# Kernel optimization log

Hardware: AMD Instinct MI355X
Metric: run time of the kernel (lower is better)

## Reference

```python
import jax, jax.numpy as jnp
import numpy as np

NH, NKV, HD = 16, 4, 64   # n_heads, n_kv_heads, head_dim
N_REP = NH // NKV
EPS = 1e-6


def rms_norm(x, w):
    var = jnp.mean(x.astype(jnp.float32) ** 2, axis=-1, keepdims=True)
    return (x.astype(jnp.float32) * jax.lax.rsqrt(var + EPS)).astype(x.dtype) * w


def rotate_half(x):
    x1, x2 = jnp.split(x, 2, axis=-1)
    return jnp.concatenate([-x2, x1], axis=-1)


def setup_inputs() -> dict:
    key = jax.random.key(0)
    ks = jax.random.split(key, 6)
    B, S, H = 2, 2048, 2048
    x = jax.random.normal(ks[0], (B, S, H), dtype=jnp.float32)
    # RoPE tables [S, HD]
    inv_freq = 1.0 / (10000.0 ** (jnp.arange(0, HD, 2, dtype=jnp.float32) / HD))
    freqs = jnp.arange(S, dtype=jnp.float32)[:, None] * inv_freq[None, :]
    emb = jnp.concatenate([freqs, freqs], axis=-1)
    cos, sin = jnp.cos(emb), jnp.sin(emb)
    scale = 0.02
    wq = jax.random.normal(ks[1], (H, NH * HD), dtype=jnp.float32) * scale
    wk = jax.random.normal(ks[2], (H, NKV * HD), dtype=jnp.float32) * scale
    wv = jax.random.normal(ks[3], (H, NKV * HD), dtype=jnp.float32) * scale
    wo = jax.random.normal(ks[4], (NH * HD, H), dtype=jnp.float32) * scale
    q_norm_w = jnp.ones((HD,), dtype=jnp.float32)
    k_norm_w = jnp.ones((HD,), dtype=jnp.float32)
    return {"x": x, "cos": cos, "sin": sin, "wq": wq, "wk": wk, "wv": wv,
            "wo": wo, "q_norm_w": q_norm_w, "k_norm_w": k_norm_w}


def reference(x, cos, sin, wq, wk, wv, wo, q_norm_w, k_norm_w):
    B, S, H = x.shape
    # QKV projections + per-head RMSNorm on q/k
    q = rms_norm((x @ wq).reshape(B, S, NH, HD), q_norm_w)
    k = rms_norm((x @ wk).reshape(B, S, NKV, HD), k_norm_w)
    v = (x @ wv).reshape(B, S, NKV, HD)
    # RoPE (broadcast over heads)
    c = cos[None, :S, None, :]
    s = sin[None, :S, None, :]
    q = q * c + rotate_half(q) * s
    k = k * c + rotate_half(k) * s
    # prefill with S == window_size: no KV eviction, T == S -> causal mask
    k = jnp.repeat(k, N_REP, axis=2)  # [B,S,NH,HD]
    v = jnp.repeat(v, N_REP, axis=2)
    scores = jnp.einsum('bqhd,bkhd->bhqk', q, k) / jnp.sqrt(jnp.float32(HD))
    causal = jnp.triu(jnp.full((S, S), -jnp.inf, dtype=scores.dtype), 1)
    scores = scores + causal
    attn = jax.nn.softmax(scores.astype(jnp.float32), axis=-1).astype(q.dtype)
    out = jnp.einsum('bhqk,bkhd->bqhd', attn, v).reshape(B, S, NH * HD)
    return out @ wo
```

## Files before the change

### kernel.cpp

```cpp
#include <hip/hip_runtime.h>

typedef float floatx4 __attribute__((ext_vector_type(4)));
typedef __bf16 bfx8 __attribute__((ext_vector_type(8)));
typedef __bf16 bfx4 __attribute__((ext_vector_type(4)));

constexpr int B_ = 2, S_ = 2048, H_ = 2048, NH_ = 16, NKV_ = 4, HD_ = 64;
constexpr int M_ = B_ * S_;
constexpr int NQKV_ = NH_ * HD_ + 2 * NKV_ * HD_;
constexpr int HQ_ = NH_ * HD_;
constexpr int XP_ = 2112;
constexpr int AP_ = 1088;
constexpr int VP_ = 2112;
constexpr int QKV_ELEMS_ = M_ * NQKV_;
constexpr float QSCL_ = 0.125f * 1.44269504088896340736f;

#define GLB(p) ((const __attribute__((address_space(1))) void*)(p))
#define LDS(p) ((__attribute__((address_space(3))) void*)(p))

__global__ __launch_bounds__(256) void prep_kernel(const float* __restrict__ x,
                                                   const float* __restrict__ wq,
                                                   const float* __restrict__ wk,
                                                   const float* __restrict__ wv,
                                                   const float* __restrict__ wo,
                                                   __bf16* __restrict__ xbf,
                                                   __bf16* __restrict__ wqkvT,
                                                   __bf16* __restrict__ woT) {
  __shared__ float tile[32][33];
  int bid = blockIdx.x;
  if (bid < M_) {
    const float4* s = (const float4*)(x + (size_t)bid * H_);
    __bf16* d = xbf + (size_t)bid * XP_;
#pragma unroll
    for (int i = 0; i < 2; i++) {
      int c = i * 256 + threadIdx.x;
      float4 v = s[c];
      bfx4 o;
      o[0] = (__bf16)v.x; o[1] = (__bf16)v.y; o[2] = (__bf16)v.z; o[3] = (__bf16)v.w;
      *(bfx4*)(d + c * 4) = o;
    }
    return;
  }
  bid -= M_;
  const float* src; __bf16* dst; int N, dstOff, pitch, nbx;
  if (bid < 2048)      { src = wq; dst = wqkvT; N = 1024; dstOff = 0;    pitch = XP_; nbx = 32; }
  else if (bid < 2560) { bid -= 2048; src = wk; dst = wqkvT; N = 256; dstOff = 1024; pitch = XP_; nbx = 8; }
  else if (bid < 3072) { bid -= 2560; src = wv; dst = wqkvT; N = 256; dstOff = 1280; pitch = XP_; nbx = 8; }
  else                 { bid -= 3072; src = wo; dst = woT;   N = 2048; dstOff = 0;   pitch = AP_; nbx = 64; }
  int n0 = (bid % nbx) * 32, k0 = (bid / nbx) * 32;
  int tx = threadIdx.x & 31, ty = threadIdx.x >> 5;
#pragma unroll
  for (int r = 0; r < 32; r += 8)
    tile[ty + r][tx] = src[(size_t)(k0 + ty + r) * N + n0 + tx];
  __syncthreads();
#pragma unroll
  for (int r = 0; r < 32; r += 8)
    dst[(size_t)(n0 + ty + r + dstOff) * pitch + k0 + tx] = (__bf16)tile[tx][ty + r];
}

__global__ __launch_bounds__(512) void gemm_bf16_f32(const __bf16* __restrict__ A,
                                                     const __bf16* __restrict__ Bt,
                                                     float* __restrict__ C,
                                                     int M, int N, int K,
                                                     int lda, int ldb, int ldc,
                                                     unsigned long long cstride) {
  __shared__ __align__(16) __bf16 As[256 * 64];
  __shared__ __align__(16) __bf16 Bs[128 * 64];
  int wid = threadIdx.x >> 6, lane = threadIdx.x & 63;
  int l15 = lane & 15, quad = lane >> 4;
  int wm = (wid >> 1) * 64, wn = (wid & 1) * 64;
  int m0 = blockIdx.y * 256, n0 = blockIdx.x * 128;
  int kb0 = blockIdx.z * K;
  C += (size_t)blockIdx.z * cstride;
  int srow_off = lane >> 3;
  int gphys = lane & 7;
  floatx4 acc[4][4] = {};
  for (int kb = kb0; kb < kb0 + K; kb += 64) {
#pragma unroll
    for (int j = 0; j < 4; j++) {
      int rbase = j * 64 + wid * 8;
      int row = rbase + srow_off;
      int glog = gphys ^ (row & 7);
      const __bf16* ga = &A[(size_t)(m0 + row) * lda + kb + glog * 8];
      __builtin_amdgcn_global_load_lds(GLB(ga), LDS(&As[rbase * 64]), 16, 0, 0);
    }
#pragma unroll
    for (int j = 0; j < 2; j++) {
      int rbase = j * 64 + wid * 8;
      int row = rbase + srow_off;
      int glog = gphys ^ (row & 7);
      const __bf16* gb = &Bt[(size_t)(n0 + row) * ldb + kb + glog * 8];
      __builtin_amdgcn_global_load_lds(GLB(gb), LDS(&Bs[rbase * 64]), 16, 0, 0);
    }
    __syncthreads();
#pragma unroll
    for (int kk = 0; kk < 64; kk += 32) {
      int cgq = (kk >> 3) + quad;
      bfx8 af[4], bfr[4];
#pragma unroll
      for (int mi = 0; mi < 4; mi++) {
        int row = wm + mi * 16 + l15;
        af[mi] = *(const bfx8*)&As[row * 64 + (cgq ^ (row & 7)) * 8];
      }
#pragma unroll
      for (int ni = 0; ni < 4; ni++) {
        int row = wn + ni * 16 + l15;
        bfr[ni] = *(const bfx8*)&Bs[row * 64 + (cgq ^ (row & 7)) * 8];
      }
#pragma unroll
      for (int mi = 0; mi < 4; mi++)
#pragma unroll
        for (int ni = 0; ni < 4; ni++)
          acc[mi][ni] = __builtin_amdgcn_mfma_f32_16x16x32_bf16(af[mi], bfr[ni], acc[mi][ni], 0, 0, 0);
    }
    __syncthreads();
  }
#pragma unroll
  for (int mi = 0; mi < 4; mi++)
#pragma unroll
    for (int ni = 0; ni < 4; ni++) {
      int row = m0 + wm + mi * 16 + quad * 4;
      int coln = n0 + wn + ni * 16 + l15;
#pragma unroll
      for (int r = 0; r < 4; r++)
        C[(size_t)(row + r) * ldc + coln] = acc[mi][ni][r];
    }
}

__global__ __launch_bounds__(256) void norm_rope_kernel(const float* __restrict__ qkv,
                                                        const float* __restrict__ cosT,
                                                        const float* __restrict__ sinT,
                                                        const float* __restrict__ qw,
                                                        const float* __restrict__ kw,
                                                        __bf16* __restrict__ Qo,
                                                        __bf16* __restrict__ Ko,
                                                        __bf16* __restrict__ VTo) {
  int s = blockIdx.x, b = blockIdx.y;
  int wid = threadIdx.x >> 6, lane = threadIdx.x & 63;
  const float* rowp = qkv + (size_t)(b * S_ + s) * NQKV_;
  const float* rowp2 = rowp + QKV_ELEMS_;
  float c = cosT[s * HD_ + lane];
  float sn = sinT[s * HD_ + lane];
#pragma unroll
  for (int it = 0; it < 5; it++) {
    int hh = it * 4 + wid;
    int idx = hh * 64 + lane;
    float v = rowp[idx] + rowp2[idx];
    float ss = v * v;
#pragma unroll
    for (int off = 1; off < 64; off <<= 1) ss += __shfl_xor(ss, off);
    float rs = rsqrtf(ss * (1.0f / 64.0f) + 1e-6f);
    const float* w = (hh < 16) ? qw : kw;
    float nv = v * rs * w[lane];
    float other = __shfl_xor(nv, 32);
    float rot = (lane < 32) ? -other : other;
    float outv = nv * c + rot * sn;
    if (hh < 16)
      Qo[(((size_t)b * NH_ + hh) * S_ + s) * HD_ + lane] = (__bf16)(outv * QSCL_);
    else
      Ko[(((size_t)b * NKV_ + (hh - 16)) * S_ + s) * HD_ + lane] = (__bf16)outv;
  }
  {
    int idx = (20 + wid) * 64 + lane;
    float v = rowp[idx] + rowp2[idx];
    VTo[(((size_t)b * NKV_ + wid) * HD_ + lane) * VP_ + s] = (__bf16)v;
  }
}

__global__ __launch_bounds__(256, 4) void attn_kernel(const __bf16* __restrict__ Q,
                                                      const __bf16* __restrict__ Kc,
                                                      const __bf16* __restrict__ VT,
                                                      __bf16* __restrict__ Ob) {
  int px = blockIdx.x, h = blockIdx.y, b = blockIdx.z;
  int u = (px + 2 * (h & 7)) & 31;
  int qt = (((h >> 3) ^ b) & 1) ? (31 - u) : u;
  int wid = threadIdx.x >> 6, lane = threadIdx.x & 63;
  int l15 = lane & 15, quad = lane >> 4;
  int q0 = qt * 64 + wid * 16;
  int kvh = h >> 2;
  const __bf16* Qh = Q + (((size_t)b * NH_ + h) * S_ + q0) * HD_;
  const __bf16* Kh = Kc + ((size_t)b * NKV_ + kvh) * S_ * HD_;
  const __bf16* Vh = VT + ((size_t)b * NKV_ + kvh) * (size_t)HD_ * VP_;
  __shared__ __align__(16) __bf16 Ks[64][72];
  __shared__ __align__(16) __bf16 Vs[64][72];
  __shared__ __align__(16) __bf16 Pst[4][16][72];
  __bf16 (*P)[72] = Pst[wid];

  int srow = threadIdx.x >> 3;
  int scol = (threadIdx.x & 7) * 8;

  bfx8 qf0, qf1;
  {
    const __bf16* qp = Qh + l15 * HD_ + quad * 8;
    qf0 = *(const bfx8*)qp;
    qf1 = *(const bfx8*)(qp + 32);
  }
  floatx4 oacc[4] = {};
  float ps = 0.f;
  int ntiles = qt + 1;
  bfx8 kpre0, kpre1, vpre0, vpre1;
  kpre0 = *(const bfx8*)&Kh[(size_t)srow * HD_ + scol];
  kpre1 = *(const bfx8*)&Kh[(size_t)(srow + 32) * HD_ + scol];
  vpre0 = *(const bfx8*)&Vh[(size_t)srow * VP_ + scol];
  vpre1 = *(const bfx8*)&Vh[(size_t)(srow + 32) * VP_ + scol];
  for (int kt = 0; kt < ntiles; kt++) {
    int kv0 = kt * 64;
    __syncthreads();
    *(bfx8*)&Ks[srow][scol] = kpre0;
    *(bfx8*)&Ks[srow + 32][scol] = kpre1;
    *(bfx8*)&Vs[srow][scol] = vpre0;
    *(bfx8*)&Vs[srow + 32][scol] = vpre1;
    __syncthreads();
    if (kt + 1 < ntiles) {
      int kn = kv0 + 64;
      kpre0 = *(const bfx8*)&Kh[(size_t)(kn + srow) * HD_ + scol];
      kpre1 = *(const bfx8*)&Kh[(size_t)(kn + srow + 32) * HD_ + scol];
      vpre0 = *(const bfx8*)&Vh[(size_t)srow * VP_ + kn + scol];
      vpre1 = *(const bfx8*)&Vh[(size_t)(srow + 32) * VP_ + kn + scol];
    }
    floatx4 sf[4];
    __builtin_amdgcn_s_setprio(1);
#pragma unroll
    for (int nt = 0; nt < 4; nt++) {
      bfx8 kf0 = *(const bfx8*)&Ks[nt * 16 + l15][quad * 8];
      bfx8 kf1 = *(const bfx8*)&Ks[nt * 16 + l15][32 + quad * 8];
      floatx4 z = {0.f, 0.f, 0.f, 0.f};
      z = __builtin_amdgcn_mfma_f32_16x16x32_bf16(kf0, qf0, z, 0, 0, 0);
      sf[nt] = __builtin_amdgcn_mfma_f32_16x16x32_bf16(kf1, qf1, z, 0, 0, 0);
    }
    __builtin_amdgcn_s_setprio(0);
    if (kt + 1 < ntiles) {
#pragma unroll
      for (int nt = 0; nt < 4; nt++) {
        bfx4 pk;
#pragma unroll
        for (int r = 0; r < 4; r++) {
          float p = exp2f(sf[nt][r]);
          ps += p;
          pk[r] = (__bf16)p;
        }
        *(bfx4*)&P[l15][nt * 16 + quad * 4] = pk;
      }
    } else {
      int dq = q0 - kv0;
#pragma unroll
      for (int nt = 0; nt < 4; nt++) {
        bfx4 pk;
#pragma unroll
        for (int r = 0; r < 4; r++) {
          int kvrel = nt * 16 + quad * 4 + r;
          float p = exp2f(sf[nt][r]);
          p = (kvrel - l15 > dq) ? 0.f : p;
          ps += p;
          pk[r] = (__bf16)p;
        }
        *(bfx4*)&P[l15][nt * 16 + quad * 4] = pk;
      }
    }
    bfx8 pa0 = *(const bfx8*)&P[l15][quad * 8];
    bfx8 pa1 = *(const bfx8*)&P[l15][32 + quad * 8];
    __builtin_amdgcn_s_setprio(1);
#pragma unroll
    for (int ot = 0; ot < 4; ot++) {
      bfx8 vf0 = *(const bfx8*)&Vs[ot * 16 + l15][quad * 8];
      bfx8 vf1 = *(const bfx8*)&Vs[ot * 16 + l15][32 + quad * 8];
      oacc[ot] = __builtin_amdgcn_mfma_f32_16x16x32_bf16(pa0, vf0, oacc[ot], 0, 0, 0);
      oacc[ot] = __builtin_amdgcn_mfma_f32_16x16x32_bf16(pa1, vf1, oacc[ot], 0, 0, 0);
    }
    __builtin_amdgcn_s_setprio(0);
  }
  ps += __shfl_xor(ps, 16);
  ps += __shfl_xor(ps, 32);
  float rl[4];
#pragma unroll
  for (int r = 0; r < 4; r++) rl[r] = 1.0f / __shfl(ps, quad * 4 + r);
#pragma unroll
  for (int ot = 0; ot < 4; ot++)
#pragma unroll
    for (int r = 0; r < 4; r++) {
      float val = oacc[ot][r] * rl[r];
      Ob[((size_t)b * S_ + q0 + quad * 4 + r) * AP_ + h * HD_ + ot * 16 + l15] = (__bf16)val;
    }
}

extern "C" void kernel_launch(void* const* d_in, const int* in_sizes, int n_in,
                              void* d_out, int out_size, void* d_ws, size_t ws_size,
                              hipStream_t stream) {
  const float* x   = (const float*)d_in[0];
  const float* cosT = (const float*)d_in[1];
  const float* sinT = (const float*)d_in[2];
  const float* wq  = (const float*)d_in[3];
  const float* wk  = (const float*)d_in[4];
  const float* wv  = (const float*)d_in[5];
  const float* wo  = (const float*)d_in[6];
  const float* qw  = (const float*)d_in[7];
  const float* kw  = (const float*)d_in[8];
  float* out = (float*)d_out;

  char* w = (char*)d_ws;
  __bf16* xbf   = (__bf16*)(w);
  __bf16* Qb    = (__bf16*)(w);
  __bf16* Kb    = (__bf16*)(w + 8388608);
  __bf16* VTb   = (__bf16*)(w + 10485760);
  __bf16* wqkvT = (__bf16*)(w + 17301504);
  __bf16* woT   = (__bf16*)(w + 23789568);
  float*  qkv   = (float*) (w + 28246016);
  __bf16* attnO = (__bf16*)(w + 28246016);

  prep_kernel<<<M_ + 5120, 256, 0, stream>>>(x, wq, wk, wv, wo, xbf, wqkvT, woT);
  gemm_bf16_f32<<<dim3(NQKV_ / 128, M_ / 256, 2), 512, 0, stream>>>(
      xbf, wqkvT, qkv, M_, NQKV_, H_ / 2, XP_, XP_, NQKV_, (unsigned long long)QKV_ELEMS_);
  norm_rope_kernel<<<dim3(S_, B_), 256, 0, stream>>>(qkv, cosT, sinT, qw, kw, Qb, Kb, VTb);
  attn_kernel<<<dim3(32, NH_, B_), 256, 0, stream>>>(Qb, Kb, VTb, attnO);
  gemm_bf16_f32<<<dim3(H_ / 128, M_ / 256, 1), 512, 0, stream>>>(
      attnO, woT, out, M_, H_, HQ_, AP_, AP_, H_, 0ull);
}
```

Baseline: 225.9 us.

## Enlarge attention query tile to 128 rows with XOR-swizzled K/V shared memory

```diff
diff --git a/kernel.cpp b/kernel.cpp
--- a/kernel.cpp
+++ b/kernel.cpp
@@ -166,119 +166,146 @@
   }
 }
 
-__global__ __launch_bounds__(256, 4) void attn_kernel(const __bf16* __restrict__ Q,
+__global__ __launch_bounds__(256, 2) void attn_kernel(const __bf16* __restrict__ Q,
                                                       const __bf16* __restrict__ Kc,
                                                       const __bf16* __restrict__ VT,
                                                       __bf16* __restrict__ Ob) {
   int px = blockIdx.x, h = blockIdx.y, b = blockIdx.z;
-  int u = (px + 2 * (h & 7)) & 31;
-  int qt = (((h >> 3) ^ b) & 1) ? (31 - u) : u;
+  int u = (px + 2 * (h & 7)) & 15;
+  int qt = (((h >> 3) ^ b) & 1) ? (15 - u) : u;
   int wid = threadIdx.x >> 6, lane = threadIdx.x & 63;
   int l15 = lane & 15, quad = lane >> 4;
-  int q0 = qt * 64 + wid * 16;
+  int q0w = qt * 128 + wid * 32;
   int kvh = h >> 2;
-  const __bf16* Qh = Q + (((size_t)b * NH_ + h) * S_ + q0) * HD_;
+  const __bf16* Qh = Q + (((size_t)b * NH_ + h) * S_ + q0w) * HD_;
   const __bf16* Kh = Kc + ((size_t)b * NKV_ + kvh) * S_ * HD_;
   const __bf16* Vh = VT + ((size_t)b * NKV_ + kvh) * (size_t)HD_ * VP_;
-  __shared__ __align__(16) __bf16 Ks[64][72];
-  __shared__ __align__(16) __bf16 Vs[64][72];
-  __shared__ __align__(16) __bf16 Pst[4][16][72];
+  __shared__ __align__(16) __bf16 Ks[64][64];
+  __shared__ __align__(16) __bf16 Vs[64][64];
+  __shared__ __align__(16) __bf16 Pst[4][32][72];
   __bf16 (*P)[72] = Pst[wid];
 
   int srow = threadIdx.x >> 3;
-  int scol = (threadIdx.x & 7) * 8;
-
-  bfx8 qf0, qf1;
+  int sg   = threadIdx.x & 7;
+  int pcol = (sg ^ (srow & 7)) * 8;
+
+  bfx8 qf0, qf1, qf2, qf3;
   {
     const __bf16* qp = Qh + l15 * HD_ + quad * 8;
     qf0 = *(const bfx8*)qp;
     qf1 = *(const bfx8*)(qp + 32);
-  }
-  floatx4 oacc[4] = {};
-  float ps = 0.f;
-  int ntiles = qt + 1;
+    qf2 = *(const bfx8*)(qp + 16 * HD_);
+    qf3 = *(const bfx8*)(qp + 16 * HD_ + 32);
+  }
+  floatx4 oacc0[4] = {}, oacc1[4] = {};
+  float ps0 = 0.f, ps1 = 0.f;
+  int ntiles = 2 * qt + 2;
+  int ktm = 2 * qt + (wid >> 1);
+  int dq0 = (wid & 1) * 32;
+  int dq1 = dq0 + 16;
+
   bfx8 kpre0, kpre1, vpre0, vpre1;
-  kpre0 = *(const bfx8*)&Kh[(size_t)srow * HD_ + scol];
-  kpre1 = *(const bfx8*)&Kh[(size_t)(srow + 32) * HD_ + scol];
-  vpre0 = *(const bfx8*)&Vh[(size_t)srow * VP_ + scol];
-  vpre1 = *(const bfx8*)&Vh[(size_t)(srow + 32) * VP_ + scol];
+  kpre0 = *(const bfx8*)&Kh[(size_t)srow * HD_ + sg * 8];
+  kpre1 = *(const bfx8*)&Kh[(size_t)(srow + 32) * HD_ + sg * 8];
+  vpre0 = *(const bfx8*)&Vh[(size_t)srow * VP_ + sg * 8];
+  vpre1 = *(const bfx8*)&Vh[(size_t)(srow + 32) * VP_ + sg * 8];
   for (int kt = 0; kt < ntiles; kt++) {
     int kv0 = kt * 64;
     __syncthreads();
-    *(bfx8*)&Ks[srow][scol] = kpre0;
-    *(bfx8*)&Ks[srow + 32][scol] = kpre1;
-    *(bfx8*)&Vs[srow][scol] = vpre0;
-    *(bfx8*)&Vs[srow + 32][scol] = vpre1;
+    *(bfx8*)&Ks[srow][pcol] = kpre0;
+    *(bfx8*)&Ks[srow + 32][pcol] = kpre1;
+    *(bfx8*)&Vs[srow][pcol] = vpre0;
+    *(bfx8*)&Vs[srow + 32][pcol] = vpre1;
     __syncthreads();
     if (kt + 1 < ntiles) {
       int kn = kv0 + 64;
-      kpre0 = *(const bfx8*)&Kh[(size_t)(kn + srow) * HD_ + scol];
-      kpre1 = *(const bfx8*)&Kh[(size_t)(kn + srow + 32) * HD_ + scol];
-      vpre0 = *(const bfx8*)&Vh[(size_t)srow * VP_ + kn + scol];
-      vpre1 = *(const bfx8*)&Vh[(size_t)(srow + 32) * VP_ + kn + scol];
-    }
-    floatx4 sf[4];
-    __builtin_amdgcn_s_setprio(1);
+      kpre0 = *(const bfx8*)&Kh[(size_t)(kn + srow) * HD_ + sg * 8];
+      kpre1 = *(const bfx8*)&Kh[(size_t)(kn + srow + 32) * HD_ + sg * 8];
+      vpre0 = *(const bfx8*)&Vh[(size_t)srow * VP_ + kn + sg * 8];
+      vpre1 = *(const bfx8*)&Vh[(size_t)(srow + 32) * VP_ + kn + sg * 8];
+    }
+    if (kt > ktm) continue;
+
+    floatx4 sf0[4], sf1[4];
 #pragma unroll
     for (int nt = 0; nt < 4; nt++) {
-      bfx8 kf0 = *(const bfx8*)&Ks[nt * 16 + l15][quad * 8];
-      bfx8 kf1 = *(const bfx8*)&Ks[nt * 16 + l15][32 + quad * 8];
-      floatx4 z = {0.f, 0.f, 0.f, 0.f};
-      z = __builtin_amdgcn_mfma_f32_16x16x32_bf16(kf0, qf0, z, 0, 0, 0);
-      sf[nt] = __builtin_amdgcn_mfma_f32_16x16x32_bf16(kf1, qf1, z, 0, 0, 0);
-    }
-    __builtin_amdgcn_s_setprio(0);
-    if (kt + 1 < ntiles) {
+      int r = nt * 16 + l15;
+      int g0 = (quad ^ (r & 7)) * 8;
+      bfx8 kf0 = *(const bfx8*)&Ks[r][g0];
+      bfx8 kf1 = *(const bfx8*)&Ks[r][g0 ^ 32];
+      floatx4 z0 = {0.f, 0.f, 0.f, 0.f}, z1 = {0.f, 0.f, 0.f, 0.f};
+      z0 = __builtin_amdgcn_mfma_f32_16x16x32_bf16(kf0, qf0, z0, 0, 0, 0);
+      sf0[nt] = __builtin_amdgcn_mfma_f32_16x16x32_bf16(kf1, qf1, z0, 0, 0, 0);
+      z1 = __builtin_amdgcn_mfma_f32_16x16x32_bf16(kf0, qf2, z1, 0, 0, 0);
+      sf1[nt] = __builtin_amdgcn_mfma_f32_16x16x32_bf16(kf1, qf3, z1, 0, 0, 0);
+    }
+    if (kt < ktm) {
 #pragma unroll
       for (int nt = 0; nt < 4; nt++) {
-        bfx4 pk;
+        bfx4 pk0, pk1;
 #pragma unroll
         for (int r = 0; r < 4; r++) {
-          float p = exp2f(sf[nt][r]);
-          ps += p;
-          pk[r] = (__bf16)p;
+          float p0 = exp2f(sf0[nt][r]);
+          float p1 = exp2f(sf1[nt][r]);
+          ps0 += p0; ps1 += p1;
+          pk0[r] = (__bf16)p0; pk1[r] = (__bf16)p1;
         }
-        *(bfx4*)&P[l15][nt * 16 + quad * 4] = pk;
+        *(bfx4*)&P[l15][nt * 16 + quad * 4] = pk0;
+        *(bfx4*)&P[16 + l15][nt * 16 + quad * 4] = pk1;
       }
     } else {
-      int dq = q0 - kv0;
 #pragma unroll
       for (int nt = 0; nt < 4; nt++) {
-        bfx4 pk;
+        bfx4 pk0, pk1;
 #pragma unroll
         for (int r = 0; r < 4; r++) {
           int kvrel = nt * 16 + quad * 4 + r;
-          float p = exp2f(sf[nt][r]);
-          p = (kvrel - l15 > dq) ? 0.f : p;
-          ps += p;
-          pk[r] = (__bf16)p;
+          float p0 = exp2f(sf0[nt][r]);
+          float p1 = exp2f(sf1[nt][r]);
+          p0 = (kvrel - l15 > dq0) ? 0.f : p0;
+          p1 = (kvrel - l15 > dq1) ? 0.f : p1;
+          ps0 += p0; ps1 += p1;
+          pk0[r] = (__bf16)p0; pk1[r] = (__bf16)p1;
         }
-        *(bfx4*)&P[l15][nt * 16 + quad * 4] = pk;
+        *(bfx4*)&P[l15][nt * 16 + quad * 4] = pk0;
+        *(bfx4*)&P[16 + l15][nt * 16 + quad * 4] = pk1;
       }
     }
-    bfx8 pa0 = *(const bfx8*)&P[l15][quad * 8];
-    bfx8 pa1 = *(const bfx8*)&P[l15][32 + quad * 8];
-    __builtin_amdgcn_s_setprio(1);
+    bfx8 pa00 = *(const bfx8*)&P[l15][quad * 8];
+    bfx8 pa01 = *(const bfx8*)&P[l15][32 + quad * 8];
+    bfx8 pa10 = *(const bfx8*)&P[16 + l15][quad * 8];
+    bfx8 pa11 = *(const bfx8*)&P[16 + l15][32 + quad * 8];
 #pragma unroll
     for (int ot = 0; ot < 4; ot++) {
-      bfx8 vf0 = *(const bfx8*)&Vs[ot * 16 + l15][quad * 8];
-      bfx8 vf1 = *(const bfx8*)&Vs[ot * 16 + l15][32 + quad * 8];
-      oacc[ot] = __builtin_amdgcn_mfma_f32_16x16x32_bf16(pa0, vf0, oacc[ot], 0, 0, 0);
-      oacc[ot] = __builtin_amdgcn_mfma_f32_16x16x32_bf16(pa1, vf1, oacc[ot], 0, 0, 0);
-    }
-    __builtin_amdgcn_s_setprio(0);
-  }
-  ps += __shfl_xor(ps, 16);
-  ps += __shfl_xor(ps, 32);
-  float rl[4];
-#pragma unroll
-  for (int r = 0; r < 4; r++) rl[r] = 1.0f / __shfl(ps, quad * 4 + r);
+      int d = ot * 16 + l15;
+      int g0 = (quad ^ (d & 7)) * 8;
+      bfx8 vf0 = *(const bfx8*)&Vs[d][g0];
+      bfx8 vf1 = *(const bfx8*)&Vs[d][g0 ^ 32];
+      oacc0[ot] = __builtin_amdgcn_mfma_f32_16x16x32_bf16(pa00, vf0, oacc0[ot], 0, 0, 0);
+      oacc0[ot] = __builtin_amdgcn_mfma_f32_16x16x32_bf16(pa01, vf1, oacc0[ot], 0, 0, 0);
+      oacc1[ot] = __builtin_amdgcn_mfma_f32_16x16x32_bf16(pa10, vf0, oacc1[ot], 0, 0, 0);
+      oacc1[ot] = __builtin_amdgcn_mfma_f32_16x16x32_bf16(pa11, vf1, oacc1[ot], 0, 0, 0);
+    }
+  }
+  ps0 += __shfl_xor(ps0, 16);
+  ps0 += __shfl_xor(ps0, 32);
+  ps1 += __shfl_xor(ps1, 16);
+  ps1 += __shfl_xor(ps1, 32);
+  float rl0[4], rl1[4];
+#pragma unroll
+  for (int r = 0; r < 4; r++) {
+    rl0[r] = 1.0f / __shfl(ps0, quad * 4 + r);
+    rl1[r] = 1.0f / __shfl(ps1, quad * 4 + r);
+  }
 #pragma unroll
   for (int ot = 0; ot < 4; ot++)
 #pragma unroll
     for (int r = 0; r < 4; r++) {
-      float val = oacc[ot][r] * rl[r];
-      Ob[((size_t)b * S_ + q0 + quad * 4 + r) * AP_ + h * HD_ + ot * 16 + l15] = (__bf16)val;
+      float v0 = oacc0[ot][r] * rl0[r];
+      float v1 = oacc1[ot][r] * rl1[r];
+      size_t col = h * HD_ + ot * 16 + l15;
+      Ob[((size_t)b * S_ + q0w + quad * 4 + r) * AP_ + col] = (__bf16)v0;
+      Ob[((size_t)b * S_ + q0w + 16 + quad * 4 + r) * AP_ + col] = (__bf16)v1;
     }
 }
 
@@ -310,7 +337,7 @@
   gemm_bf16_f32<<<dim3(NQKV_ / 128, M_ / 256, 2), 512, 0, stream>>>(
       xbf, wqkvT, qkv, M_, NQKV_, H_ / 2, XP_, XP_, NQKV_, (unsigned long long)QKV_ELEMS_);
   norm_rope_kernel<<<dim3(S_, B_), 256, 0, stream>>>(qkv, cosT, sinT, qw, kw, Qb, Kb, VTb);
-  attn_kernel<<<dim3(32, NH_, B_), 256, 0, stream>>>(Qb, Kb, VTb, attnO);
+  attn_kernel<<<dim3(S_ / 128, NH_, B_), 256, 0, stream>>>(Qb, Kb, VTb, attnO);
   gemm_bf16_f32<<<dim3(H_ / 128, M_ / 256, 1), 512, 0, stream>>>(
       attnO, woT, out, M_, H_, HQ_, AP_, AP_, H_, 0ull);
 }
```

After: 225.4 us. About the same (-0.2%).
